# Kernel optimization log

Hardware: AMD Instinct MI355X
Metric: run time of the kernel (lower is better)

## Reference

```python
import jax, jax.numpy as jnp
import numpy as np

EPS = 1e-5
N_NODES = 100000

def _glorot(key, shape):
    lim = float(np.sqrt(6.0 / (shape[0] + shape[1])))
    return jax.random.uniform(key, shape, jnp.float32, -lim, lim)

def setup_inputs() -> dict:
    key = jax.random.key(0)
    ks = jax.random.split(key, 16)
    x = jax.random.normal(ks[0], (N_NODES, 64), jnp.float32)
    edge_index = jax.random.randint(ks[1], (2, 1600000), 0, N_NODES, jnp.int64)
    chans = [64, 128, 128, 1]
    inp = {"x": x, "edge_index": edge_index}
    for i in range(3):
        ci, co = chans[i], chans[i + 1]
        inp[f"Wl{i}"] = _glorot(ks[2 + 3 * i], (ci, co))
        inp[f"bl{i}"] = jnp.zeros((co,), jnp.float32)
        inp[f"Wr{i}"] = _glorot(ks[3 + 3 * i], (ci, co))
    inp["g0"] = jnp.ones((128,), jnp.float32); inp["be0"] = jnp.zeros((128,), jnp.float32)
    inp["g1"] = jnp.ones((128,), jnp.float32); inp["be1"] = jnp.zeros((128,), jnp.float32)
    inp["wF"] = _glorot(ks[11], (1, 1))
    inp["bF"] = jnp.zeros((1,), jnp.float32)
    return inp

def _sage_conv(x, src, dst, Wl, bl, Wr):
    # mean aggregation over incoming edges (PyG SAGEConv default)
    msg = x[src]                                                   # [E, Cin]
    agg = jax.ops.segment_sum(msg, dst, num_segments=N_NODES)      # [N, Cin]
    cnt = jax.ops.segment_sum(jnp.ones((src.shape[0], 1), x.dtype), dst, num_segments=N_NODES)
    agg = agg / jnp.maximum(cnt, 1.0)
    return agg @ Wl + bl + x @ Wr

def _batchnorm(x, g, b):
    mu = jnp.mean(x, axis=0)
    var = jnp.mean(jnp.square(x - mu), axis=0)  # biased, training-mode BN
    return (x - mu) * jax.lax.rsqrt(var + EPS) * g + b

def reference(x, edge_index, Wl0, bl0, Wr0, Wl1, bl1, Wr1, Wl2, bl2, Wr2, g0, be0, g1, be1, wF, bF):
    src, dst = edge_index[0], edge_index[1]
    h = _sage_conv(x, src, dst, Wl0, bl0, Wr0)
    h = jax.nn.relu(_batchnorm(h, g0, be0))
    h = _sage_conv(h, src, dst, Wl1, bl1, Wr1)
    h = jax.nn.relu(_batchnorm(h, g1, be1))
    h = _sage_conv(h, src, dst, Wl2, bl2, Wr2)        # activation 'None', no BN
    h = h @ wF + bF                                    # final Linear(1,1)
    return jax.nn.sigmoid(h)
```

## Files before the change

kernel.cpp:

```cpp
#include <hip/hip_runtime.h>
#include <math.h>

#define BN_EPS 1e-5f
#define SCAN_CHUNK 4096

typedef __attribute__((ext_vector_type(8))) short bf16x8;
typedef __attribute__((ext_vector_type(4))) float f32x4;

__device__ __forceinline__ unsigned short f2bf(float f) {
    unsigned int u = __float_as_uint(f);
    u = (u + 0x7fffu + ((u >> 16) & 1u)) >> 16;
    return (unsigned short)u;
}
__device__ __forceinline__ float bflo(unsigned int u) { return __uint_as_float(u << 16); }
__device__ __forceinline__ float bfhi(unsigned int u) { return __uint_as_float(u & 0xffff0000u); }

template<bool BNIN>
__device__ __forceinline__ void acc2(unsigned int u, float sc0, float sh0, float sc1, float sh1,
                                     float& a0, float& a1) {
    if constexpr (BNIN) {
        a0 += fmaxf(bflo(u) * sc0 + sh0, 0.f);
        a1 += fmaxf(bfhi(u) * sc1 + sh1, 0.f);
    } else {
        a0 += bflo(u);
        a1 += bfhi(u);
    }
}

__global__ void to_bf16_k(const float* __restrict__ in, unsigned short* __restrict__ out, int n4) {
    int i = blockIdx.x * blockDim.x + threadIdx.x;
    if (i >= n4) return;
    float4 v = ((const float4*)in)[i];
    ((ushort4*)out)[i] = make_ushort4(f2bf(v.x), f2bf(v.y), f2bf(v.z), f2bf(v.w));
}

__global__ void count_edges_sliced_k(const int* __restrict__ dst, int E,
                                     int* __restrict__ cnt, int nper) {
    const int slice = blockIdx.x & 7;
    const int lo = slice * nper;
    const int hi = lo + nper;
    int i = (blockIdx.x >> 3) * blockDim.x + threadIdx.x;
    int stride = (gridDim.x >> 3) * blockDim.x;
    for (int e = i; e < E; e += stride) {
        int d = dst[e];
        if (d >= lo && d < hi) atomicAdd(&cnt[d], 1);
    }
}

__device__ __forceinline__ int wave_incl_scan(int v, int lane) {
#pragma unroll
    for (int d = 1; d < 64; d <<= 1) {
        int u = __shfl_up(v, d);
        if (lane >= d) v += u;
    }
    return v;
}

__global__ void block_sum_k(const int* __restrict__ cnt, int N, int* __restrict__ bsum) {
    const int t = threadIdx.x;
    const int base = blockIdx.x * SCAN_CHUNK;
    int s = 0;
    for (int i = t; i < SCAN_CHUNK; i += 256) {
        int idx = base + i;
        if (idx < N) s += cnt[idx];
    }
    const int lane = t & 63, wid = t >> 6;
#pragma unroll
    for (int d = 32; d; d >>= 1) s += __shfl_down(s, d);
    __shared__ int ws[4];
    if (lane == 0) ws[wid] = s;
    __syncthreads();
    if (t == 0) bsum[blockIdx.x] = ws[0] + ws[1] + ws[2] + ws[3];
}

__global__ void scan_write_k(const int* __restrict__ cnt, const int* __restrict__ bsum, int nb,
                             int N, int* __restrict__ off, int* __restrict__ cursor,
                             float* __restrict__ inv) {
    const int t = threadIdx.x;
    __shared__ int ws[4];
    __shared__ int base_s;
    if (t < 64) {
        int v = (t < nb) ? bsum[t] : 0;
        int incl = wave_incl_scan(v, t);
        if (t == blockIdx.x) base_s = incl - v;
    }
    const int base = blockIdx.x * SCAN_CHUNK;
    const int idx0 = base + t * 16;
    int pre[16];
    int s = 0;
#pragma unroll
    for (int j = 0; j < 16; ++j) {
        int i = idx0 + j;
        int c = (i < N) ? cnt[i] : 0;
        pre[j] = s;
        s += c;
    }
    const int lane = t & 63, wid = t >> 6;
    int incl = wave_incl_scan(s, lane);
    if (lane == 63) ws[wid] = incl;
    __syncthreads();
    if (t == 0) {
        int a = 0;
#pragma unroll
        for (int w = 0; w < 4; ++w) { int tmp = ws[w]; ws[w] = a; a += tmp; }
    }
    __syncthreads();
    const int tbase = base_s + (incl - s) + ws[wid];
#pragma unroll
    for (int j = 0; j < 16; ++j) {
        int i = idx0 + j;
        if (i < N) {
            int c = cnt[i];
            int o = tbase + pre[j];
            off[i] = o;
            cursor[i] = o;
            inv[i] = 1.0f / fmaxf((float)c, 1.0f);
        }
    }
}

__global__ void csr_fill_sliced_k(const int* __restrict__ src, const int* __restrict__ dst,
                                  const int* __restrict__ off, int E,
                                  int* __restrict__ cursor, int* __restrict__ csr,
                                  float slice_scale) {
    const int slice = blockIdx.x & 7;
    const int g = blockIdx.x >> 3;
    const int ng = gridDim.x >> 3;
    int i = g * blockDim.x + threadIdx.x;
    int stride = ng * blockDim.x;
    for (int e = i; e < E; e += stride) {
        int d = dst[e];
        int o = off[d];
        int s = (int)((float)o * slice_scale);
        s = s > 7 ? 7 : s;
        if (s == slice) {
            int pos = atomicAdd(&cursor[d], 1);
            csr[pos] = src[e];
        }
    }
}

__global__ void wfrag_build_k(const float* __restrict__ Wl, const float* __restrict__ Wr,
                              int CIN, int KIT, unsigned short* __restrict__ wf) {
    int t = blockIdx.x * blockDim.x + threadIdx.x;
    int lane = t & 63;
    int q = t >> 6;
    if (q >= 8 * KIT) return;
    int kit = q % KIT;
    int ct = q / KIT;
    int col = ct * 16 + (lane & 15);
    bf16x8 v;
#pragma unroll
    for (int j = 0; j < 8; ++j) {
        int kg = kit * 32 + ((lane >> 4) << 3) + j;
        float f = (kg < CIN) ? Wl[(size_t)kg * 128 + col] : Wr[(size_t)(kg - CIN) * 128 + col];
        v[j] = (short)f2bf(f);
    }
    ((bf16x8*)wf)[q * 64 + lane] = v;
}

template<int CIN, bool BNIN>
__launch_bounds__(256)
__global__ void fused_sage_k(const unsigned short* __restrict__ feat,
                             const unsigned short* __restrict__ xin,
                             const int* __restrict__ csr, const int* __restrict__ off,
                             const int* __restrict__ endp, const float* __restrict__ inv,
                             const unsigned short* __restrict__ wfrag,
                             const float* __restrict__ bl,
                             const float* __restrict__ g, const float* __restrict__ be,
                             const float* __restrict__ stats8in,
                             unsigned short* __restrict__ outb,
                             float* __restrict__ stats8out, int N) {
    constexpr int KT = 2 * CIN;
    constexpr int KIT = KT / 32;
    __shared__ unsigned short sA[32 * KT];
    __shared__ float sfinS[256];

    const int t = threadIdx.x;
    const int lane = t & 63, wave = t >> 6;
    const int rowbase = blockIdx.x * 32;
    const unsigned int* f32p = (const unsigned int*)feat;

    if constexpr (BNIN) {
        if (t < 128) {
            float s = 0.f, s2 = 0.f;
#pragma unroll
            for (int k = 0; k < 8; ++k) { s += stats8in[k * 256 + t]; s2 += stats8in[k * 256 + 128 + t]; }
            float mu = s / (float)N;
            float var = s2 / (float)N - mu * mu;
            float sc = g[t] * rsqrtf(var + BN_EPS);
            sfinS[t] = sc;
            sfinS[128 + t] = be[t] - mu * sc;
        }
        __syncthreads();
    }

    constexpr int CH8 = CIN / 8;
    for (int i = t; i < 32 * CH8; i += 256) {
        int r = i / CH8, q = i % CH8;
        if (rowbase + r < N) {
            uint4 v = ((const uint4*)(xin + (size_t)(rowbase + r) * CIN))[q];
            if constexpr (BNIN) {
                unsigned int w[4] = {v.x, v.y, v.z, v.w};
#pragma unroll
                for (int j = 0; j < 4; ++j) {
                    int c = q * 8 + 2 * j;
                    float lo = fmaxf(bflo(w[j]) * sfinS[c]     + sfinS[128 + c],     0.f);
                    float hi = fmaxf(bfhi(w[j]) * sfinS[c + 1] + sfinS[128 + c + 1], 0.f);
                    w[j] = (unsigned int)f2bf(lo) | ((unsigned int)f2bf(hi) << 16);
                }
                v = make_uint4(w[0], w[1], w[2], w[3]);
            }
            int byte = ((r * KT + CIN + q * 8) * 2) ^ ((r & 7) << 4);
            *(uint4*)((char*)sA + byte) = v;
        }
    }

    float sc0 = 1.f, sh0 = 0.f, sc1 = 1.f, sh1 = 0.f;
    if constexpr (BNIN) {
        int cc = (CIN == 128) ? (2 * lane) : (2 * (lane & 31));
        sc0 = sfinS[cc];     sh0 = sfinS[128 + cc];
        sc1 = sfinS[cc + 1]; sh1 = sfinS[128 + cc + 1];
    }

#pragma unroll
    for (int rr = 0; rr < 8; ++rr) {
        int r = wave * 8 + rr;
        int n = rowbase + r;
        if (n < N) {
            const int o = off[n], eend = endp[n];
            float a0 = 0.f, a1 = 0.f, b0f = 0.f, b1f = 0.f;
            if constexpr (CIN == 128) {
                int e = o;
                for (; e + 7 < eend; e += 8) {
                    unsigned int u0 = f32p[(size_t)csr[e]     * 64 + lane];
                    unsigned int u1 = f32p[(size_t)csr[e + 1] * 64 + lane];
                    unsigned int u2 = f32p[(size_t)csr[e + 2] * 64 + lane];
                    unsigned int u3 = f32p[(size_t)csr[e + 3] * 64 + lane];
                    unsigned int u4 = f32p[(size_t)csr[e + 4] * 64 + lane];
                    unsigned int u5 = f32p[(size_t)csr[e + 5] * 64 + lane];
                    unsigned int u6 = f32p[(size_t)csr[e + 6] * 64 + lane];
                    unsigned int u7 = f32p[(size_t)csr[e + 7] * 64 + lane];
                    acc2<BNIN>(u0, sc0, sh0, sc1, sh1, a0, a1);
                    acc2<BNIN>(u1, sc0, sh0, sc1, sh1, b0f, b1f);
                    acc2<BNIN>(u2, sc0, sh0, sc1, sh1, a0, a1);
                    acc2<BNIN>(u3, sc0, sh0, sc1, sh1, b0f, b1f);
                    acc2<BNIN>(u4, sc0, sh0, sc1, sh1, a0, a1);
                    acc2<BNIN>(u5, sc0, sh0, sc1, sh1, b0f, b1f);
                    acc2<BNIN>(u6, sc0, sh0, sc1, sh1, a0, a1);
                    acc2<BNIN>(u7, sc0, sh0, sc1, sh1, b0f, b1f);
                }
                for (; e + 3 < eend; e += 4) {
                    unsigned int u0 = f32p[(size_t)csr[e]     * 64 + lane];
                    unsigned int u1 = f32p[(size_t)csr[e + 1] * 64 + lane];
                    unsigned int u2 = f32p[(size_t)csr[e + 2] * 64 + lane];
                    unsigned int u3 = f32p[(size_t)csr[e + 3] * 64 + lane];
                    acc2<BNIN>(u0, sc0, sh0, sc1, sh1, a0, a1);
                    acc2<BNIN>(u1, sc0, sh0, sc1, sh1, b0f, b1f);
                    acc2<BNIN>(u2, sc0, sh0, sc1, sh1, a0, a1);
                    acc2<BNIN>(u3, sc0, sh0, sc1, sh1, b0f, b1f);
                }
                for (; e < eend; ++e) {
                    unsigned int u = f32p[(size_t)csr[e] * 64 + lane];
                    acc2<BNIN>(u, sc0, sh0, sc1, sh1, a0, a1);
                }
                a0 += b0f; a1 += b1f;
                float iv = inv[n];
                unsigned int pk = (unsigned int)f2bf(a0 * iv) | ((unsigned int)f2bf(a1 * iv) << 16);
                int byte = ((r * KT + 2 * lane) * 2) ^ ((r & 7) << 4);
                *(unsigned int*)((char*)sA + byte) = pk;
            } else {
                const int c = lane & 31, g2 = lane >> 5;
                int e = o + g2;
                for (; e + 14 < eend; e += 16) {
                    unsigned int u0 = f32p[(size_t)csr[e]      * 32 + c];
                    unsigned int u1 = f32p[(size_t)csr[e + 2]  * 32 + c];
                    unsigned int u2 = f32p[(size_t)csr[e + 4]  * 32 + c];
                    unsigned int u3 = f32p[(size_t)csr[e + 6]  * 32 + c];
                    unsigned int u4 = f32p[(size_t)csr[e + 8]  * 32 + c];
                    unsigned int u5 = f32p[(size_t)csr[e + 10] * 32 + c];
                    unsigned int u6 = f32p[(size_t)csr[e + 12] * 32 + c];
                    unsigned int u7 = f32p[(size_t)csr[e + 14] * 32 + c];
                    acc2<false>(u0, 0, 0, 0, 0, a0, a1);
                    acc2<false>(u1, 0, 0, 0, 0, b0f, b1f);
                    acc2<false>(u2, 0, 0, 0, 0, a0, a1);
                    acc2<false>(u3, 0, 0, 0, 0, b0f, b1f);
                    acc2<false>(u4, 0, 0, 0, 0, a0, a1);
                    acc2<false>(u5, 0, 0, 0, 0, b0f, b1f);
                    acc2<false>(u6, 0, 0, 0, 0, a0, a1);
                    acc2<false>(u7, 0, 0, 0, 0, b0f, b1f);
                }
                for (; e + 6 < eend; e += 8) {
                    unsigned int u0 = f32p[(size_t)csr[e]     * 32 + c];
                    unsigned int u1 = f32p[(size_t)csr[e + 2] * 32 + c];
                    unsigned int u2 = f32p[(size_t)csr[e + 4] * 32 + c];
                    unsigned int u3 = f32p[(size_t)csr[e + 6] * 32 + c];
                    acc2<false>(u0, 0, 0, 0, 0, a0, a1);
                    acc2<false>(u1, 0, 0, 0, 0, b0f, b1f);
                    acc2<false>(u2, 0, 0, 0, 0, a0, a1);
                    acc2<false>(u3, 0, 0, 0, 0, b0f, b1f);
                }
                for (; e < eend; e += 2) {
                    unsigned int u = f32p[(size_t)csr[e] * 32 + c];
                    acc2<false>(u, 0, 0, 0, 0, a0, a1);
                }
                a0 += b0f; a1 += b1f;
                a0 += __shfl_xor(a0, 32);
                a1 += __shfl_xor(a1, 32);
                if (g2 == 0) {
                    float iv = inv[n];
                    unsigned int pk = (unsigned int)f2bf(a0 * iv) | ((unsigned int)f2bf(a1 * iv) << 16);
                    int byte = ((r * KT + 2 * c) * 2) ^ ((r & 7) << 4);
                    *(unsigned int*)((char*)sA + byte) = pk;
                }
            }
        }
    }
    __syncthreads();

    f32x4 acc00 = {0.f,0.f,0.f,0.f}, acc01 = acc00, acc10 = acc00, acc11 = acc00;
    const int koff = (lane >> 4) << 4;
    const int swz = (lane & 7) << 4;
    const int base0 = (lane & 15) * KT * 2 + koff;
    const int base1 = (16 + (lane & 15)) * KT * 2 + koff;
    const bf16x8* wf8 = (const bf16x8*)wfrag;
    const int bq0 = (wave * 2 + 0) * KIT;
    const int bq1 = (wave * 2 + 1) * KIT;

#pragma unroll
    for (int kit = 0; kit < KIT; ++kit) {
        bf16x8 fa0 = *(const bf16x8*)((const char*)sA + ((base0 + kit * 64) ^ swz));
        bf16x8 fa1 = *(const bf16x8*)((const char*)sA + ((base1 + kit * 64) ^ swz));
        bf16x8 fb0 = wf8[(bq0 + kit) * 64 + lane];
        bf16x8 fb1 = wf8[(bq1 + kit) * 64 + lane];
        acc00 = __builtin_amdgcn_mfma_f32_16x16x32_bf16(fa0, fb0, acc00, 0, 0, 0);
        acc01 = __builtin_amdgcn_mfma_f32_16x16x32_bf16(fa0, fb1, acc01, 0, 0, 0);
        acc10 = __builtin_amdgcn_mfma_f32_16x16x32_bf16(fa1, fb0, acc10, 0, 0, 0);
        acc11 = __builtin_amdgcn_mfma_f32_16x16x32_bf16(fa1, fb1, acc11, 0, 0, 0);
    }

    const int c0 = wave * 32 + (lane & 15);
    const int c1 = c0 + 16;
    const float b0 = bl[c0], b1 = bl[c1];
    float sum0 = 0.f, sq0 = 0.f, sum1 = 0.f, sq1 = 0.f;
    const int row0base = rowbase + ((lane >> 4) << 2);
#pragma unroll
    for (int r = 0; r < 4; ++r) {
        int row0 = row0base + r, row1 = row0 + 16;
        float v00 = acc00[r] + b0, v01 = acc01[r] + b1;
        float v10 = acc10[r] + b0, v11 = acc11[r] + b1;
        if (row0 < N) {
            outb[(size_t)row0 * 128 + c0] = f2bf(v00);
            outb[(size_t)row0 * 128 + c1] = f2bf(v01);
            sum0 += v00; sq0 += v00 * v00; sum1 += v01; sq1 += v01 * v01;
        }
        if (row1 < N) {
            outb[(size_t)row1 * 128 + c0] = f2bf(v10);
            outb[(size_t)row1 * 128 + c1] = f2bf(v11);
            sum0 += v10; sq0 += v10 * v10; sum1 += v11; sq1 += v11 * v11;
        }
    }
#pragma unroll
    for (int m = 16; m < 64; m <<= 1) {
        sum0 += __shfl_xor(sum0, m); sq0 += __shfl_xor(sq0, m);
        sum1 += __shfl_xor(sum1, m); sq1 += __shfl_xor(sq1, m);
    }
    if (lane < 16) {
        float* st = stats8out + (blockIdx.x & 7) * 256;
        atomicAdd(&st[c0], sum0);
        atomicAdd(&st[128 + c0], sq0);
        atomicAdd(&st[c1], sum1);
        atomicAdd(&st[128 + c1], sq1);
    }
}

__global__ void bn_finalize8_k(const float* __restrict__ g, const float* __restrict__ be,
                               const float* __restrict__ stats8, float* __restrict__ sfin, int N) {
    int c = threadIdx.x;
    if (c < 128) {
        float s = 0.f, s2 = 0.f;
#pragma unroll
        for (int k = 0; k < 8; ++k) { s += stats8[k * 256 + c]; s2 += stats8[k * 256 + 128 + c]; }
        float mu = s / (float)N;
        float var = s2 / (float)N - mu * mu;
        float sc = g[c] * rsqrtf(var + BN_EPS);
        sfin[c] = sc;
        sfin[128 + c] = be[c] - mu * sc;
    }
}

__global__ void bn_apply_p_k(unsigned short* __restrict__ hb, const float* __restrict__ sfin,
                             const float* __restrict__ Wl2, float* __restrict__ p, int N) {
    const int lane = threadIdx.x & 63;
    const int n = (int)((blockIdx.x * (long long)blockDim.x + threadIdx.x) >> 6);
    if (n >= N) return;
    const float2 sc = ((const float2*)sfin)[lane];
    const float2 sh = ((const float2*)(sfin + 128))[lane];
    const float2 w  = ((const float2*)Wl2)[lane];
    unsigned int u = ((unsigned int*)(hb + (size_t)n * 128))[lane];
    float vx = fmaxf(bflo(u) * sc.x + sh.x, 0.f);
    float vy = fmaxf(bfhi(u) * sc.y + sh.y, 0.f);
    ((unsigned int*)(hb + (size_t)n * 128))[lane] = (unsigned int)f2bf(vx) | ((unsigned int)f2bf(vy) << 16);
    float s = vx * w.x + vy * w.y;
#pragma unroll
    for (int o = 32; o; o >>= 1) s += __shfl_down(s, o);
    if (lane == 0) p[n] = s;
}

__global__ void layer2_final_k(const unsigned short* __restrict__ hb, const float* __restrict__ p,
                               const int* __restrict__ csr, const int* __restrict__ off,
                               const int* __restrict__ endp, const float* __restrict__ inv,
                               const float* __restrict__ Wr2, const float* __restrict__ bl2,
                               const float* __restrict__ wF, const float* __restrict__ bF,
                               float* __restrict__ out, int N) {
    const int lane = threadIdx.x & 63;
    const int n = (int)((blockIdx.x * (long long)blockDim.x + threadIdx.x) >> 6);
    if (n >= N) return;
    float2 w = ((const float2*)Wr2)[lane];
    unsigned int u = ((const unsigned int*)(hb + (size_t)n * 128))[lane];
    float dotp = bflo(u) * w.x + bfhi(u) * w.y;
    float ps = 0.f;
    const int o = off[n], e_end = endp[n];
    for (int e = o + lane; e < e_end; e += 64) ps += p[csr[e]];
    float s = dotp + ps * inv[n];
#pragma unroll
    for (int ow = 32; ow; ow >>= 1) s += __shfl_down(s, ow);
    if (lane == 0) {
        float z = (s + bl2[0]) * wF[0] + bF[0];
        out[n] = 1.f / (1.f + expf(-z));
    }
}

extern "C" void kernel_launch(void* const* d_in, const int* in_sizes, int n_in,
                              void* d_out, int out_size, void* d_ws, size_t ws_size,
                              hipStream_t stream) {
    const float* x   = (const float*)d_in[0];
    const int*   ei  = (const int*)d_in[1];
    const int E = in_sizes[1] / 2;
    const int N = in_sizes[0] / 64;
    const int* src = ei;
    const int* dst = ei + E;
    const float* Wl0 = (const float*)d_in[2];
    const float* bl0 = (const float*)d_in[3];
    const float* Wr0 = (const float*)d_in[4];
    const float* Wl1 = (const float*)d_in[5];
    const float* bl1 = (const float*)d_in[6];
    const float* Wr1 = (const float*)d_in[7];
    const float* Wl2 = (const float*)d_in[8];
    const float* bl2 = (const float*)d_in[9];
    const float* Wr2 = (const float*)d_in[10];
    const float* g0  = (const float*)d_in[11];
    const float* be0 = (const float*)d_in[12];
    const float* g1  = (const float*)d_in[13];
    const float* be1 = (const float*)d_in[14];
    const float* wF  = (const float*)d_in[15];
    const float* bF  = (const float*)d_in[16];

    char* wp = (char*)d_ws;
    unsigned short* h0   = (unsigned short*)wp;  wp += (size_t)N * 128 * 2;
    unsigned short* h1   = (unsigned short*)wp;  wp += (size_t)N * 128 * 2;
    unsigned short* xb   = (unsigned short*)wp;  wp += (size_t)N * 64 * 2;
    int*   cnt    = (int*)wp;    wp += (size_t)N * 4;
    int*   off    = (int*)wp;    wp += (size_t)N * 4;
    int*   cursor = (int*)wp;    wp += (size_t)N * 4;
    float* inv    = (float*)wp;  wp += (size_t)N * 4;
    int*   csr    = (int*)wp;    wp += (size_t)E * 4;
    float* stats8a = (float*)wp; wp += 2048 * 4;
    float* stats8b = (float*)wp; wp += 2048 * 4;
    float* sfin1   = (float*)wp; wp += 256 * 4;
    int*   bsum    = (int*)wp;   wp += 64 * 4;
    unsigned short* wf0 = (unsigned short*)wp; wp += 8 * 4 * 64 * 8 * 2;
    unsigned short* wf1 = (unsigned short*)wp; wp += 8 * 8 * 64 * 8 * 2;
    float* p = (float*)cnt;
    float* out = (float*)d_out;

    const int gemm_grid = (N + 31) / 32;
    const int wave_grid = (N + 3) / 4;
    const int nb = (N + SCAN_CHUNK - 1) / SCAN_CHUNK;

    wfrag_build_k<<<(8 * 4 * 64 + 255) / 256, 256, 0, stream>>>(Wl0, Wr0, 64, 4, wf0);
    wfrag_build_k<<<(8 * 8 * 64 + 255) / 256, 256, 0, stream>>>(Wl1, Wr1, 128, 8, wf1);
    to_bf16_k<<<(N * 16 + 255) / 256, 256, 0, stream>>>(x, xb, N * 16);
    hipMemsetAsync(stats8a, 0, (2048 + 2048) * sizeof(float), stream);

    hipMemsetAsync(cnt, 0, (size_t)N * sizeof(int), stream);
    count_edges_sliced_k<<<2048, 256, 0, stream>>>(dst, E, cnt, (N + 7) / 8);
    block_sum_k<<<nb, 256, 0, stream>>>(cnt, N, bsum);
    scan_write_k<<<nb, 256, 0, stream>>>(cnt, bsum, nb, N, off, cursor, inv);
    csr_fill_sliced_k<<<2048, 256, 0, stream>>>(src, dst, off, E, cursor, csr, 8.0f / (float)E);

    fused_sage_k<64, false><<<gemm_grid, 256, 0, stream>>>(
        xb, xb, csr, off, cursor, inv, wf0, bl0, nullptr, nullptr, nullptr, h0, stats8a, N);

    fused_sage_k<128, true><<<gemm_grid, 256, 0, stream>>>(
        h0, h0, csr, off, cursor, inv, wf1, bl1, g0, be0, stats8a, h1, stats8b, N);

    bn_finalize8_k<<<1, 128, 0, stream>>>(g1, be1, stats8b, sfin1, N);
    bn_apply_p_k<<<wave_grid, 256, 0, stream>>>(h1, sfin1, Wl2, p, N);

    layer2_final_k<<<wave_grid, 256, 0, stream>>>(h1, p, csr, off, cursor, inv,
                                                  Wr2, bl2, wF, bF, out, N);
}
```

Measured before the change: 397.3 us.

## Pre-bucketize edges by destination range before CSR fill

Replaces the sliced CSR fill, in which each of 8 block groups scanned every edge and kept only its slice, with a two-pass scheme. A bucketize kernel groups each 2048-edge chunk by destination bucket in shared memory and writes (src,dst) pairs contiguously per bucket. The fill kernel then reads only its bucket's range. This drops the 8x redundant reads of src, dst and off, but adds an 8-byte-per-edge intermediate buffer plus one extra write and read pass.

```diff
diff --git a/kernel.cpp b/kernel.cpp
--- a/kernel.cpp
+++ b/kernel.cpp
@@ -3,6 +3,7 @@
 
 #define BN_EPS 1e-5f
 #define SCAN_CHUNK 4096
+#define BCHUNK 2048
 
 typedef __attribute__((ext_vector_type(8))) short bf16x8;
 typedef __attribute__((ext_vector_type(4))) float f32x4;
@@ -119,24 +120,75 @@
     }
 }
 
-__global__ void csr_fill_sliced_k(const int* __restrict__ src, const int* __restrict__ dst,
-                                  const int* __restrict__ off, int E,
-                                  int* __restrict__ cursor, int* __restrict__ csr,
-                                  float slice_scale) {
-    const int slice = blockIdx.x & 7;
+__global__ void bucket_base_k(const int* __restrict__ off, int N, int E, int nper,
+                              int* __restrict__ bbase, int* __restrict__ bcur) {
+    int b = threadIdx.x;
+    if (b < 9) {
+        int node = b * nper;
+        int v = (node < N) ? off[node] : E;
+        bbase[b] = v;
+        if (b < 8) bcur[b] = v;
+    }
+}
+
+__global__ void bucketize_k(const int* __restrict__ src, const int* __restrict__ dst,
+                            int E, int nper, int* __restrict__ bcur, uint2* __restrict__ ebuf) {
+    __shared__ int hist[8], lofs[8], gofs[8], cpos[8];
+    __shared__ uint2 buf[BCHUNK];
+    const int t = threadIdx.x;
+    const int base = blockIdx.x * BCHUNK;
+    if (base >= E) return;
+    const int chunk = min(BCHUNK, E - base);
+
+    if (t < 8) hist[t] = 0;
+    __syncthreads();
+
+    int my_d[8], my_s[8], my_b[8];
+#pragma unroll
+    for (int j = 0; j < 8; ++j) {
+        int e = base + j * 256 + t;
+        if (j * 256 + t < chunk) {
+            my_d[j] = dst[e];
+            my_s[j] = src[e];
+            my_b[j] = my_d[j] / nper;
+            atomicAdd(&hist[my_b[j]], 1);
+        } else my_b[j] = -1;
+    }
+    __syncthreads();
+    if (t == 0) {
+        int a = 0;
+#pragma unroll
+        for (int b = 0; b < 8; ++b) { lofs[b] = a; cpos[b] = a; a += hist[b]; }
+    }
+    __syncthreads();
+    if (t < 8) gofs[t] = hist[t] ? atomicAdd(&bcur[t], hist[t]) : 0;
+    __syncthreads();
+#pragma unroll
+    for (int j = 0; j < 8; ++j) {
+        if (my_b[j] >= 0) {
+            int pos = atomicAdd(&cpos[my_b[j]], 1);
+            buf[pos] = make_uint2((unsigned)my_s[j], (unsigned)my_d[j]);
+        }
+    }
+    __syncthreads();
+    for (int i = t; i < chunk; i += 256) {
+        int b = 0;
+#pragma unroll
+        for (int bb = 1; bb < 8; ++bb) if (i >= lofs[bb]) b = bb;
+        ebuf[gofs[b] + (i - lofs[b])] = buf[i];
+    }
+}
+
+__global__ void csr_fill_bucketed_k(const uint2* __restrict__ ebuf, const int* __restrict__ bbase,
+                                    int* __restrict__ cursor, int* __restrict__ csr) {
+    const int s = blockIdx.x & 7;
     const int g = blockIdx.x >> 3;
     const int ng = gridDim.x >> 3;
-    int i = g * blockDim.x + threadIdx.x;
-    int stride = ng * blockDim.x;
-    for (int e = i; e < E; e += stride) {
-        int d = dst[e];
-        int o = off[d];
-        int s = (int)((float)o * slice_scale);
-        s = s > 7 ? 7 : s;
-        if (s == slice) {
-            int pos = atomicAdd(&cursor[d], 1);
-            csr[pos] = src[e];
-        }
+    const int lo = bbase[s], hi = bbase[s + 1];
+    for (int i = lo + g * blockDim.x + threadIdx.x; i < hi; i += ng * blockDim.x) {
+        uint2 v = ebuf[i];
+        int pos = atomicAdd(&cursor[(int)v.y], 1);
+        csr[pos] = (int)v.x;
     }
 }
 
@@ -465,10 +517,13 @@
     int*   cursor = (int*)wp;    wp += (size_t)N * 4;
     float* inv    = (float*)wp;  wp += (size_t)N * 4;
     int*   csr    = (int*)wp;    wp += (size_t)E * 4;
+    uint2* ebuf   = (uint2*)wp;  wp += (size_t)E * 8;
     float* stats8a = (float*)wp; wp += 2048 * 4;
     float* stats8b = (float*)wp; wp += 2048 * 4;
     float* sfin1   = (float*)wp; wp += 256 * 4;
     int*   bsum    = (int*)wp;   wp += 64 * 4;
+    int*   bbase   = (int*)wp;   wp += 16 * 4;
+    int*   bcur    = (int*)wp;   wp += 16 * 4;
     unsigned short* wf0 = (unsigned short*)wp; wp += 8 * 4 * 64 * 8 * 2;
     unsigned short* wf1 = (unsigned short*)wp; wp += 8 * 8 * 64 * 8 * 2;
     float* p = (float*)cnt;
@@ -477,6 +532,8 @@
     const int gemm_grid = (N + 31) / 32;
     const int wave_grid = (N + 3) / 4;
     const int nb = (N + SCAN_CHUNK - 1) / SCAN_CHUNK;
+    const int nper = (N + 7) / 8;
+    const int nchunks = (E + BCHUNK - 1) / BCHUNK;
 
     wfrag_build_k<<<(8 * 4 * 64 + 255) / 256, 256, 0, stream>>>(Wl0, Wr0, 64, 4, wf0);
     wfrag_build_k<<<(8 * 8 * 64 + 255) / 256, 256, 0, stream>>>(Wl1, Wr1, 128, 8, wf1);
@@ -484,10 +541,12 @@
     hipMemsetAsync(stats8a, 0, (2048 + 2048) * sizeof(float), stream);
 
     hipMemsetAsync(cnt, 0, (size_t)N * sizeof(int), stream);
-    count_edges_sliced_k<<<2048, 256, 0, stream>>>(dst, E, cnt, (N + 7) / 8);
+    count_edges_sliced_k<<<2048, 256, 0, stream>>>(dst, E, cnt, nper);
     block_sum_k<<<nb, 256, 0, stream>>>(cnt, N, bsum);
     scan_write_k<<<nb, 256, 0, stream>>>(cnt, bsum, nb, N, off, cursor, inv);
-    csr_fill_sliced_k<<<2048, 256, 0, stream>>>(src, dst, off, E, cursor, csr, 8.0f / (float)E);
+    bucket_base_k<<<1, 16, 0, stream>>>(off, N, E, nper, bbase, bcur);
+    bucketize_k<<<nchunks, 256, 0, stream>>>(src, dst, E, nper, bcur, ebuf);
+    csr_fill_bucketed_k<<<2048, 256, 0, stream>>>(ebuf, bbase, cursor, csr);
 
     fused_sage_k<64, false><<<gemm_grid, 256, 0, stream>>>(
         xb, xb, csr, off, cursor, inv, wf0, bl0, nullptr, nullptr, nullptr, h0, stats8a, N);
```

Result: no change. 391.6 us (-1.4%).
